# Kernel tuning notes

Hardware: AMD Instinct MI355X
Metric: run time of the kernel (lower is better)

## Reference

```python
import jax, jax.numpy as jnp
import numpy as np

N_FILES = 256      # number of files (segments)
LINES = 128        # lines per file
T = N_FILES * LINES  # total lines = 32768
D_ENC = 768        # CodeBERT hidden size
HID = 256          # GCN hidden_dim
SD = 128           # shared_dim
PD = 128           # private_dim
WINDOW = 2         # line-graph window
S_AM = 30.0        # AM-Softmax scale
M_AM = 0.35        # AM-Softmax margin


def _build_edges():
    # build_line_graph: connect lines within a file at offsets 1..WINDOW, both directions
    idx = np.arange(T)
    srcs, dsts = [], []
    for off in range(1, WINDOW + 1):
        m = (idx % LINES) + off < LINES  # j stays inside the same file
        i = idx[m]; j = i + off
        srcs += [i, j]; dsts += [j, i]
    return np.stack([np.concatenate(srcs), np.concatenate(dsts)]).astype(np.int32)


def setup_inputs() -> dict:
    key = jax.random.key(0)
    ks = jax.random.split(key, 18)
    std = 0.02
    inp = {
        "line_emb": jax.random.normal(ks[0], (T, D_ENC), jnp.float32),
        "W1": jax.random.normal(ks[1], (D_ENC, HID), jnp.float32) * std,
        "b1": jnp.zeros((HID,), jnp.float32),
        "W2": jax.random.normal(ks[2], (HID, HID), jnp.float32) * std,
        "b2": jnp.zeros((HID,), jnp.float32),
        "attn_w": jax.random.normal(ks[3], (HID, 1), jnp.float32) * std,
        "attn_b": jnp.zeros((1,), jnp.float32),
        "Ws": jax.random.normal(ks[4], (HID, SD), jnp.float32) * std,
        "bs": jnp.zeros((SD,), jnp.float32),
        "Wp": jax.random.normal(ks[5], (HID, PD), jnp.float32) * std,
        "bp": jnp.zeros((PD,), jnp.float32),
        "cls_w": jax.random.normal(ks[6], (SD, 2), jnp.float32) * std,
        "Wd1": jax.random.normal(ks[7], (SD, SD), jnp.float32) * std,
        "bd1": jnp.zeros((SD,), jnp.float32),
        "Wd2": jax.random.normal(ks[8], (SD, 2), jnp.float32) * std,
        "bd2": jnp.zeros((2,), jnp.float32),
        "line_ptr": jnp.arange(0, T + 1, LINES, dtype=jnp.int32),
        "edge_index": jnp.asarray(_build_edges()),
        "file_labels": jax.random.randint(ks[9], (N_FILES,), 0, 2, jnp.int32),
    }
    return inp


def _l2norm(x):
    return x / jnp.maximum(jnp.linalg.norm(x, axis=1, keepdims=True), 1e-12)


def _gcn(x, W, b, src, dst, n):
    sl = jnp.arange(n, dtype=src.dtype)
    src = jnp.concatenate([src, sl]); dst = jnp.concatenate([dst, sl])
    deg = jax.ops.segment_sum(jnp.ones_like(src, jnp.float32), dst, num_segments=n)
    norm = jax.lax.rsqrt(deg[src] * deg[dst])  # [E+n]
    h = x @ W                                   # [n, out]
    msg = h[src] * norm[:, None]
    return jax.ops.segment_sum(msg, dst, num_segments=n) + b


def reference(line_emb, W1, b1, W2, b2, attn_w, attn_b, Ws, bs, Wp, bp,
              cls_w, Wd1, bd1, Wd2, bd2, line_ptr, edge_index, file_labels):
    n = line_emb.shape[0]
    n_files = line_ptr.shape[0] - 1
    src, dst = edge_index[0], edge_index[1]

    h = jax.nn.relu(_gcn(line_emb, W1, b1, src, dst, n))
    h = _gcn(h, W2, b2, src, dst, n)               # [T, HID]

    # ragged per-file softmax attention pooling
    seg = jnp.searchsorted(line_ptr, jnp.arange(n, dtype=line_ptr.dtype), side="right") - 1
    logits = (h @ attn_w).squeeze(-1) + attn_b[0]  # [T]
    seg_max = jax.ops.segment_max(logits, seg, num_segments=n_files)
    e = jnp.exp(logits - seg_max[seg])
    denom = jax.ops.segment_sum(e, seg, num_segments=n_files)
    att_weights = e / denom[seg]
    h_file = jax.ops.segment_sum(att_weights[:, None] * h, seg, num_segments=n_files)  # [N, HID]

    # disentangle heads
    z_shared = h_file @ Ws + bs
    z_private = h_file @ Wp + bp

    # AM-Softmax classifier (labels given -> subtract margin on true class)
    cos = _l2norm(z_shared) @ (cls_w / jnp.maximum(jnp.linalg.norm(cls_w, axis=0, keepdims=True), 1e-12))
    onehot = jax.nn.one_hot(file_labels, 2, dtype=cos.dtype)
    logits_cls = S_AM * (cos - M_AM * onehot)

    # orthogonality loss
    corr = _l2norm(z_shared).T @ _l2norm(z_private)
    ortho = jnp.linalg.norm(corr)

    # domain discriminator (GRL is identity in forward)
    domain_logits = jax.nn.relu(z_shared @ Wd1 + bd1) @ Wd2 + bd2

    return (logits_cls, h_file, z_shared, z_private, att_weights, domain_logits, ortho)
```

## Files before the change

### kernel.cpp

```cpp
#include <hip/hip_runtime.h>


typedef __attribute__((ext_vector_type(8))) short bf16x8;
typedef __attribute__((ext_vector_type(4))) short bf16x4;
typedef __attribute__((ext_vector_type(4))) float f32x4;
typedef __attribute__((ext_vector_type(8))) float f32x8;

__device__ __forceinline__ unsigned short f2bf(float f) {
  union { float f; unsigned int i; } v; v.f = f;
  unsigned int r = v.i + 0x7FFFu + ((v.i >> 16) & 1u);
  return (unsigned short)(r >> 16);
}
__device__ __forceinline__ float bf2f(unsigned short u) {
  union { unsigned int i; float f; } v; v.i = ((unsigned int)u) << 16; return v.f;
}
__device__ __forceinline__ float cvt4dot(bf16x4 v, f32x4* o) {
  (*o)[0] = bf2f(((unsigned short*)&v)[0]); (*o)[1] = bf2f(((unsigned short*)&v)[1]);
  (*o)[2] = bf2f(((unsigned short*)&v)[2]); (*o)[3] = bf2f(((unsigned short*)&v)[3]);
  return 0.f;
}
__device__ __forceinline__ int degf(int p) {
  return 5 - (p < 2 ? 2 - p : 0) - (p > 125 ? p - 125 : 0);
}
__device__ __forceinline__ float wsum(float v) {
#pragma unroll
  for (int o = 1; o < 64; o <<= 1) v += __shfl_xor(v, o);
  return v;
}

__global__ void prep_weights(const float* __restrict__ W1, const float* __restrict__ W2,
                             const float* __restrict__ Ws, const float* __restrict__ Wp,
                             const float* __restrict__ Wd1,
                             unsigned short* __restrict__ W1t, unsigned short* __restrict__ W2t,
                             unsigned short* __restrict__ WsbG, unsigned short* __restrict__ WpbG,
                             unsigned short* __restrict__ Wd1bG) {
  __shared__ float tile[32][33];
  int id = blockIdx.x;
  int tx = threadIdx.x, ty = threadIdx.y;
  if (id >= 256) {
    int id2 = id - 256;
    const float* src; unsigned short* dst; int blk;
    if (id2 < 32)      { src = Ws;  dst = WsbG;  blk = id2; }
    else if (id2 < 64) { src = Wp;  dst = WpbG;  blk = id2 - 32; }
    else               { src = Wd1; dst = Wd1bG; blk = id2 - 64; }
    int tid = ty * 32 + tx;
    int e0 = blk * 1024 + tid * 4;
    f32x4 v = *(const f32x4*)&src[e0];
    unsigned short o[4];
#pragma unroll
    for (int j = 0; j < 4; ++j) o[j] = f2bf(v[j]);
    *(bf16x4*)&dst[e0] = *(bf16x4*)o;
    return;
  }
  const float* src; unsigned short* dst; int R, C, bx, by;
  if (id < 192) { src = W1; dst = W1t; R = 768; C = 256; bx = (id % 8) * 32; by = (id / 8) * 32; }
  else { id -= 192; src = W2; dst = W2t; R = 256; C = 256; bx = (id % 8) * 32; by = (id / 8) * 32; }
#pragma unroll
  for (int j = 0; j < 32; j += 8)
    tile[ty + j][tx] = src[(by + ty + j) * C + bx + tx];
  __syncthreads();
#pragma unroll
  for (int j = 0; j < 32; j += 8)
    dst[(bx + ty + j) * R + by + tx] = f2bf(tile[tx][ty + j]);
}

__global__ __launch_bounds__(1024) void mega(const float* __restrict__ A,
    const unsigned short* __restrict__ W1t, const float* __restrict__ b1,
    const unsigned short* __restrict__ W2t, const float* __restrict__ b2,
    const float* __restrict__ attn_w, const float* __restrict__ attn_b,
    const unsigned short* __restrict__ WsbG, const float* __restrict__ bs,
    const unsigned short* __restrict__ WpbG, const float* __restrict__ bp,
    const float* __restrict__ cls_w, const int* __restrict__ labels,
    const unsigned short* __restrict__ Wd1bG, const float* __restrict__ bd1,
    const float* __restrict__ Wd2, const float* __restrict__ bd2,
    float* __restrict__ out) {
  __shared__ __align__(16) char lds[131072];
  unsigned short* sA1 = (unsigned short*)lds;
  unsigned short* sB1 = (unsigned short*)(lds + 32768);
  unsigned short* H1  = (unsigned short*)lds;
  unsigned short* G1L = (unsigned short*)(lds + 65536);
  unsigned short* sB2 = (unsigned short*)lds;
  unsigned short* H2  = (unsigned short*)lds;
  unsigned short* hB  = (unsigned short*)(lds + 65536);
  unsigned short* Wlo = (unsigned short*)lds;
  unsigned short* Whi = (unsigned short*)(lds + 65536);
  __shared__ float awS[256];
  __shared__ float lgS[128];
  __shared__ float redM[64];
  __shared__ float scr[1024];
  __shared__ float hfS[256];
  __shared__ float zsS[128], znS[128];
  __shared__ float redS[16];

  const int t = threadIdx.x;
  const int wave = t >> 6, lane = t & 63;
  const int wr = wave >> 2, wc = wave & 3;
  const int file = blockIdx.x;
  const long rowA = (long)file * 128;

  if (t < 256) awS[t] = attn_w[t];

  f32x4 acc[2][4];
#pragma unroll
  for (int m = 0; m < 2; ++m)
#pragma unroll
    for (int n = 0; n < 4; ++n) acc[m][n] = (f32x4)0.0f;

  const int arow = t >> 3, acol = (t & 7) * 8;
  const int aswz = arow * 64 + (acol ^ ((arow & 7) << 3));
  f32x8 areg;
#define ISSUE_A1(kt) areg = *(const f32x8*)&A[(rowA + arow) * 768 + (kt) * 64 + acol]
#define WRITE_A1(buf) { unsigned short u[8];                                      \
    _Pragma("unroll") for (int j = 0; j < 8; ++j) u[j] = f2bf(areg[j]);           \
    *(bf16x8*)&sA1[(buf) * 8192 + aswz] = *(bf16x8*)u; }
#define ISSUE_B1(kt, buf) _Pragma("unroll") for (int it = 0; it < 2; ++it) {      \
    int flat = (it * 1024 + t) * 8;                                               \
    int n = flat >> 6, k = flat & 63;                                             \
    const unsigned short* g = W1t + n * 768 + (kt) * 64 + (k ^ ((n & 7) << 3));   \
    __builtin_amdgcn_global_load_lds(                                             \
        (const __attribute__((address_space(1))) unsigned int*)g,                 \
        (__attribute__((address_space(3))) unsigned int*)                         \
            &sB1[(buf) * 16384 + (it * 16 + wave) * 512], 16, 0, 0); }

  ISSUE_A1(0); ISSUE_B1(0, 0); WRITE_A1(0);
  __syncthreads();
  for (int kt = 0; kt < 12; ++kt) {
    const int cur = kt & 1, nxt = cur ^ 1;
    if (kt + 1 < 12) { ISSUE_A1(kt + 1); ISSUE_B1(kt + 1, nxt); }
#pragma unroll
    for (int kk = 0; kk < 2; ++kk) {
      const int kb = kk * 32 + (lane >> 4) * 8;
      bf16x8 af[2], bfr[4];
#pragma unroll
      for (int m = 0; m < 2; ++m) {
        int r = wr * 32 + m * 16 + (lane & 15);
        af[m] = *(const bf16x8*)&sA1[cur * 8192 + r * 64 + (kb ^ ((r & 7) << 3))];
      }
#pragma unroll
      for (int n = 0; n < 4; ++n) {
        int r = wc * 64 + n * 16 + (lane & 15);
        bfr[n] = *(const bf16x8*)&sB1[cur * 16384 + r * 64 + (kb ^ ((r & 7) << 3))];
      }
#pragma unroll
      for (int m = 0; m < 2; ++m)
#pragma unroll
        for (int n = 0; n < 4; ++n)
          acc[m][n] = __builtin_amdgcn_mfma_f32_16x16x32_bf16(af[m], bfr[n], acc[m][n], 0, 0, 0);
    }
    if (kt + 1 < 12) WRITE_A1(nxt);
    __syncthreads();
  }
#pragma unroll
  for (int m = 0; m < 2; ++m)
#pragma unroll
    for (int n = 0; n < 4; ++n) {
      int r = wr * 32 + m * 16 + (lane >> 4) * 4;
      int c = wc * 64 + n * 16 + (lane & 15);
#pragma unroll
      for (int j = 0; j < 4; ++j) H1[(r + j) * 256 + c] = f2bf(acc[m][n][j]);
    }
  __syncthreads();
#pragma unroll
  for (int it = 0; it < 8; ++it) {
    int g = it * 1024 + t;
    int l = g >> 6, c0 = (g & 63) * 4;
    int dl = degf(l);
    f32x4 s = (f32x4)0.0f;
#pragma unroll
    for (int o = -2; o <= 2; ++o) {
      int q = l + o;
      if (q < 0 || q > 127) continue;
      float w = __frsqrt_rn((float)(dl * degf(q)));
      bf16x4 hv4 = *(const bf16x4*)&H1[q * 256 + c0];
      f32x4 hv; cvt4dot(hv4, &hv);
      s += w * hv;
    }
    f32x4 b = *(const f32x4*)&b1[c0];
    unsigned short o4[4];
#pragma unroll
    for (int j = 0; j < 4; ++j) o4[j] = f2bf(fmaxf(s[j] + b[j], 0.f));
    *(bf16x4*)&G1L[l * 256 + (c0 ^ ((l & 7) << 3))] = *(bf16x4*)o4;
  }
  __syncthreads();

#pragma unroll
  for (int m = 0; m < 2; ++m)
#pragma unroll
    for (int n = 0; n < 4; ++n) acc[m][n] = (f32x4)0.0f;
#define ISSUE_B2(kt, buf) _Pragma("unroll") for (int it = 0; it < 2; ++it) {      \
    int flat = (it * 1024 + t) * 8;                                               \
    int n = flat >> 6, k = flat & 63;                                             \
    const unsigned short* g = W2t + n * 256 + (kt) * 64 + (k ^ ((n & 7) << 3));   \
    __builtin_amdgcn_global_load_lds(                                             \
        (const __attribute__((address_space(1))) unsigned int*)g,                 \
        (__attribute__((address_space(3))) unsigned int*)                         \
            &sB2[(buf) * 16384 + (it * 16 + wave) * 512], 16, 0, 0); }

  ISSUE_B2(0, 0);
  __syncthreads();
  for (int kt = 0; kt < 4; ++kt) {
    const int cur = kt & 1, nxt = cur ^ 1;
    if (kt + 1 < 4) ISSUE_B2(kt + 1, nxt);
#pragma unroll
    for (int kk = 0; kk < 2; ++kk) {
      const int kb = kk * 32 + (lane >> 4) * 8;
      bf16x8 af[2], bfr[4];
#pragma unroll
      for (int m = 0; m < 2; ++m) {
        int r = wr * 32 + m * 16 + (lane & 15);
        int col = kt * 64 + kb;
        af[m] = *(const bf16x8*)&G1L[r * 256 + (col ^ ((r & 7) << 3))];
      }
#pragma unroll
      for (int n = 0; n < 4; ++n) {
        int r = wc * 64 + n * 16 + (lane & 15);
        bfr[n] = *(const bf16x8*)&sB2[cur * 16384 + r * 64 + (kb ^ ((r & 7) << 3))];
      }
#pragma unroll
      for (int m = 0; m < 2; ++m)
#pragma unroll
        for (int n = 0; n < 4; ++n)
          acc[m][n] = __builtin_amdgcn_mfma_f32_16x16x32_bf16(af[m], bfr[n], acc[m][n], 0, 0, 0);
    }
    __syncthreads();
  }
#pragma unroll
  for (int m = 0; m < 2; ++m)
#pragma unroll
    for (int n = 0; n < 4; ++n) {
      int r = wr * 32 + m * 16 + (lane >> 4) * 4;
      int c = wc * 64 + n * 16 + (lane & 15);
#pragma unroll
      for (int j = 0; j < 4; ++j) H2[(r + j) * 256 + c] = f2bf(acc[m][n][j]);
    }
  __syncthreads();
#pragma unroll
  for (int it = 0; it < 8; ++it) {
    int g = it * 1024 + t;
    int l = g >> 6, c0 = (g & 63) * 4;
    int dl = degf(l);
    f32x4 s = (f32x4)0.0f;
#pragma unroll
    for (int o = -2; o <= 2; ++o) {
      int q = l + o;
      if (q < 0 || q > 127) continue;
      float w = __frsqrt_rn((float)(dl * degf(q)));
      bf16x4 hv4 = *(const bf16x4*)&H2[q * 256 + c0];
      f32x4 hv; cvt4dot(hv4, &hv);
      s += w * hv;
    }
    f32x4 b = *(const f32x4*)&b2[c0];
    unsigned short o4[4];
#pragma unroll
    for (int j = 0; j < 4; ++j) o4[j] = f2bf(s[j] + b[j]);
    *(bf16x4*)&hB[l * 256 + c0] = *(bf16x4*)o4;
  }
  __syncthreads();
#define ISSUE_WB(srcG, dstL, rounds) _Pragma("unroll") for (int it = 0; it < (rounds); ++it) { \
    const unsigned short* g = (srcG) + (it * 1024 + t) * 8;                        \
    __builtin_amdgcn_global_load_lds(                                              \
        (const __attribute__((address_space(1))) unsigned int*)g,                  \
        (__attribute__((address_space(3))) unsigned int*)                          \
            &(dstL)[(it * 16 + wave) * 512], 16, 0, 0); }
  ISSUE_WB(WsbG, Wlo, 4);

  {
    int l = t >> 3, p = t & 7;
    float part = 0.f;
#pragma unroll 4
    for (int j = 0; j < 32; ++j) {
      int c = p * 32 + ((j + 4 * p + l) & 31);
      part += bf2f(hB[l * 256 + c]) * awS[c];
    }
    part += __shfl_xor(part, 1);
    part += __shfl_xor(part, 2);
    part += __shfl_xor(part, 4);
    if (p == 0) lgS[l] = part + attn_b[0];
  }
  __syncthreads();
  if (t < 64) redM[t] = fmaxf(lgS[t], lgS[t + 64]);
  __syncthreads();
  for (int s = 32; s > 0; s >>= 1) {
    if (t < s) redM[t] = fmaxf(redM[t], redM[t + s]);
    __syncthreads();
  }
  float mx = redM[0];
  __syncthreads();
  if (t < 128) lgS[t] = expf(lgS[t] - mx);
  __syncthreads();
  if (t < 64) redM[t] = lgS[t] + lgS[t + 64];
  __syncthreads();
  for (int s = 32; s > 0; s >>= 1) {
    if (t < s) redM[t] += redM[t + s];
    __syncthreads();
  }
  float dn = redM[0];
  __syncthreads();
  if (t < 128) {
    float w = lgS[t] / dn;
    lgS[t] = w;
    out[131584 + file * 128 + t] = w;
  }
  __syncthreads();
  {
    int c = t & 255, grp = t >> 8;
    float s = 0.f;
    for (int l = grp * 32; l < grp * 32 + 32; ++l) s += lgS[l] * bf2f(hB[l * 256 + c]);
    scr[grp * 256 + c] = s;
  }
  __syncthreads();
  if (t < 256) {
    float tot = scr[t] + scr[256 + t] + scr[512 + t] + scr[768 + t];
    hfS[t] = tot;
    out[512 + file * 256 + t] = tot;
  }
  __syncthreads();

  ISSUE_WB(WpbG, Whi, 4);
  {
    int g = t >> 7, j = t & 127;
    float s = 0.f;
#pragma unroll 8
    for (int c = g * 32; c < g * 32 + 32; ++c) s += hfS[c] * bf2f(Wlo[c * 128 + j]);
    scr[g * 128 + j] = s;
  }
  __syncthreads();
  ISSUE_WB(Wd1bG, Wlo, 2);
  if (t < 128) {
    float zs = bs[t];
#pragma unroll
    for (int g = 0; g < 8; ++g) zs += scr[g * 128 + t];
    zsS[t] = zs;
    out[66048 + file * 128 + t] = zs;
    float s = wsum(zs * zs);
    if (lane == 0) redS[wave] = s;
  }
  __syncthreads();
  if (t == 0) redS[8] = fmaxf(sqrtf(redS[0] + redS[1]), 1e-12f);
  {
    int g = t >> 7, j = t & 127;
    float s = 0.f;
#pragma unroll 8
    for (int c = g * 32; c < g * 32 + 32; ++c) s += hfS[c] * bf2f(Whi[c * 128 + j]);
    scr[g * 128 + j] = s;
  }
  __syncthreads();
  if (t < 128) {
    znS[t] = zsS[t] / redS[8];
  } else if (t < 256) {
    int j = t - 128;
    float zp = bp[j];
#pragma unroll
    for (int g = 0; g < 8; ++g) zp += scr[g * 128 + j];
    out[98816 + file * 128 + j] = zp;
  }
  __syncthreads();
  {
    int j = t & 127;
    if (t < 512) {
      float v;
      if (t < 128)       v = znS[j] * cls_w[j * 2 + 0];
      else if (t < 256)  v = znS[j] * cls_w[j * 2 + 1];
      else if (t < 384)  { float w0 = cls_w[j * 2 + 0]; v = w0 * w0; }
      else               { float w1 = cls_w[j * 2 + 1]; v = w1 * w1; }
      float s = wsum(v);
      if (lane == 0) redS[wave] = s;
    }
  }
  __syncthreads();
  if (t == 0) {
    float d0 = redS[0] + redS[1], d1 = redS[2] + redS[3];
    float n0 = fmaxf(sqrtf(redS[4] + redS[5]), 1e-12f);
    float n1 = fmaxf(sqrtf(redS[6] + redS[7]), 1e-12f);
    int lab = labels[file];
    out[file * 2 + 0] = 30.0f * (d0 / n0 - 0.35f * (lab == 0 ? 1.f : 0.f));
    out[file * 2 + 1] = 30.0f * (d1 / n1 - 0.35f * (lab == 1 ? 1.f : 0.f));
  }
  __syncthreads();
  {
    int g = t >> 7, j = t & 127;
    float s = 0.f;
#pragma unroll 8
    for (int a = g * 16; a < g * 16 + 16; ++a) s += zsS[a] * bf2f(Wlo[a * 128 + j]);
    scr[g * 128 + j] = s;
  }
  __syncthreads();
  if (t < 128) {
    float dd = bd1[t];
#pragma unroll
    for (int g = 0; g < 8; ++g) dd += scr[g * 128 + t];
    dd = fmaxf(dd, 0.f);
    float s0 = wsum(dd * Wd2[t * 2 + 0]);
    if (lane == 0) redS[wave] = s0;
    float s1 = wsum(dd * Wd2[t * 2 + 1]);
    if (lane == 0) redS[4 + wave] = s1;
  }
  __syncthreads();
  if (t == 0) {
    out[164352 + file * 2 + 0] = redS[0] + redS[1] + bd2[0];
    out[164352 + file * 2 + 1] = redS[4] + redS[5] + bd2[1];
  }
#undef ISSUE_A1
#undef WRITE_A1
#undef ISSUE_B1
#undef ISSUE_B2
#undef ISSUE_WB
}

__global__ __launch_bounds__(128) void znorm(const float* __restrict__ out,
                                             float* __restrict__ zsn,
                                             float* __restrict__ zpn) {
  const int f = blockIdx.x, j = threadIdx.x;
  __shared__ float red[128];
  float zs = out[66048 + f * 128 + j];
  float zp = out[98816 + f * 128 + j];
  red[j] = zs * zs; __syncthreads();
  for (int s = 64; s > 0; s >>= 1) { if (j < s) red[j] += red[j + s]; __syncthreads(); }
  float ns = sqrtf(red[0]); __syncthreads();
  zsn[f * 128 + j] = zs / fmaxf(ns, 1e-12f);
  red[j] = zp * zp; __syncthreads();
  for (int s = 64; s > 0; s >>= 1) { if (j < s) red[j] += red[j + s]; __syncthreads(); }
  float np = sqrtf(red[0]); __syncthreads();
  zpn[f * 128 + j] = zp / fmaxf(np, 1e-12f);
}

__global__ __launch_bounds__(128) void ortho_partial(const float* __restrict__ zsn,
                                                     const float* __restrict__ zpn,
                                                     float* __restrict__ partial) {
  const int a = blockIdx.x, b = threadIdx.x;
  float s = 0.f;
  for (int f = 0; f < 256; ++f) s += zsn[f * 128 + a] * zpn[f * 128 + b];
  __shared__ float red[128];
  red[b] = s * s; __syncthreads();
  for (int st = 64; st > 0; st >>= 1) { if (b < st) red[b] += red[b + st]; __syncthreads(); }
  if (b == 0) partial[a] = red[0];
}

__global__ __launch_bounds__(128) void ortho_final(const float* __restrict__ partial,
                                                   float* __restrict__ out) {
  const int t = threadIdx.x;
  __shared__ float red[128];
  red[t] = partial[t]; __syncthreads();
  for (int st = 64; st > 0; st >>= 1) { if (t < st) red[t] += red[t + st]; __syncthreads(); }
  if (t == 0) out[164864] = sqrtf(red[0]);
}

extern "C" void kernel_launch(void* const* d_in, const int* in_sizes, int n_in,
                              void* d_out, int out_size, void* d_ws, size_t ws_size,
                              hipStream_t stream) {
  const float* line_emb = (const float*)d_in[0];
  const float* W1     = (const float*)d_in[1];
  const float* b1     = (const float*)d_in[2];
  const float* W2     = (const float*)d_in[3];
  const float* b2     = (const float*)d_in[4];
  const float* attn_w = (const float*)d_in[5];
  const float* attn_b = (const float*)d_in[6];
  const float* Ws     = (const float*)d_in[7];
  const float* bs     = (const float*)d_in[8];
  const float* Wp     = (const float*)d_in[9];
  const float* bp     = (const float*)d_in[10];
  const float* cls_w  = (const float*)d_in[11];
  const float* Wd1    = (const float*)d_in[12];
  const float* bd1    = (const float*)d_in[13];
  const float* Wd2    = (const float*)d_in[14];
  const float* bd2    = (const float*)d_in[15];
  const int* labels   = (const int*)d_in[18];

  char* ws = (char*)d_ws;
  unsigned short* W1t  = (unsigned short*)(ws + 0);
  unsigned short* W2t  = (unsigned short*)(ws + 393216);
  float* zsn           = (float*)(ws + 524288);
  float* zpn           = (float*)(ws + 655360);
  float* partial       = (float*)(ws + 786432);
  unsigned short* WsbG = (unsigned short*)(ws + 1048576);
  unsigned short* WpbG = (unsigned short*)(ws + 1114112);
  unsigned short* Wd1bG= (unsigned short*)(ws + 1179648);
  float* out           = (float*)d_out;

  prep_weights<<<dim3(336), dim3(32, 8), 0, stream>>>(W1, W2, Ws, Wp, Wd1,
                                                      W1t, W2t, WsbG, WpbG, Wd1bG);
  mega<<<dim3(256), dim3(1024), 0, stream>>>(line_emb, W1t, b1, W2t, b2,
                                             attn_w, attn_b, WsbG, bs, WpbG, bp,
                                             cls_w, labels, Wd1bG, bd1, Wd2, bd2, out);
  znorm<<<dim3(256), dim3(128), 0, stream>>>(out, zsn, zpn);
  ortho_partial<<<dim3(128), dim3(128), 0, stream>>>(zsn, zpn, partial);
  ortho_final<<<dim3(1), dim3(128), 0, stream>>>(partial, out);
}
```

Measured before the change: 73.18 us.

## Fuse z normalisation into mega kernel, swizzle hB, and use wave-shuffle reductions

```diff
diff --git a/kernel.cpp b/kernel.cpp
--- a/kernel.cpp
+++ b/kernel.cpp
@@ -73,6 +73,7 @@
     const float* __restrict__ cls_w, const int* __restrict__ labels,
     const unsigned short* __restrict__ Wd1bG, const float* __restrict__ bd1,
     const float* __restrict__ Wd2, const float* __restrict__ bd2,
+    float* __restrict__ zsn_g, float* __restrict__ zpn_g,
     float* __restrict__ out) {
   __shared__ __align__(16) char lds[131072];
   unsigned short* sA1 = (unsigned short*)lds;
@@ -86,10 +87,10 @@
   unsigned short* Whi = (unsigned short*)(lds + 65536);
   __shared__ float awS[256];
   __shared__ float lgS[128];
-  __shared__ float redM[64];
+  __shared__ float redM[4];
   __shared__ float scr[1024];
   __shared__ float hfS[256];
-  __shared__ float zsS[128], znS[128];
+  __shared__ float zsS[128], zpS[128], znS[128];
   __shared__ float redS[16];
 
   const int t = threadIdx.x;
@@ -253,7 +254,7 @@
     unsigned short o4[4];
 #pragma unroll
     for (int j = 0; j < 4; ++j) o4[j] = f2bf(s[j] + b[j]);
-    *(bf16x4*)&hB[l * 256 + c0] = *(bf16x4*)o4;
+    *(bf16x4*)&hB[l * 256 + (c0 ^ ((l & 7) << 3))] = *(bf16x4*)o4;
   }
   __syncthreads();
 #define ISSUE_WB(srcG, dstL, rounds) _Pragma("unroll") for (int it = 0; it < (rounds); ++it) { \
@@ -266,11 +267,14 @@
 
   {
     int l = t >> 3, p = t & 7;
+    const int sw = (l & 7) << 3;
     float part = 0.f;
-#pragma unroll 4
-    for (int j = 0; j < 32; ++j) {
-      int c = p * 32 + ((j + 4 * p + l) & 31);
-      part += bf2f(hB[l * 256 + c]) * awS[c];
+#pragma unroll
+    for (int j = 0; j < 4; ++j) {
+      int c0 = p * 32 + j * 8;
+      bf16x8 hv = *(const bf16x8*)&hB[l * 256 + (c0 ^ sw)];
+#pragma unroll
+      for (int e = 0; e < 8; ++e) part += bf2f(((unsigned short*)&hv)[e]) * awS[c0 + e];
     }
     part += __shfl_xor(part, 1);
     part += __shfl_xor(part, 2);
@@ -278,24 +282,22 @@
     if (p == 0) lgS[l] = part + attn_b[0];
   }
   __syncthreads();
-  if (t < 64) redM[t] = fmaxf(lgS[t], lgS[t + 64]);
-  __syncthreads();
-  for (int s = 32; s > 0; s >>= 1) {
-    if (t < s) redM[t] = fmaxf(redM[t], redM[t + s]);
-    __syncthreads();
-  }
+  if (wave == 0) {
+    float m0 = fmaxf(lgS[lane], lgS[lane + 64]);
+#pragma unroll
+    for (int o = 1; o < 64; o <<= 1) m0 = fmaxf(m0, __shfl_xor(m0, o));
+    if (lane == 0) redM[0] = m0;
+  }
+  __syncthreads();
   float mx = redM[0];
-  __syncthreads();
   if (t < 128) lgS[t] = expf(lgS[t] - mx);
   __syncthreads();
-  if (t < 64) redM[t] = lgS[t] + lgS[t + 64];
-  __syncthreads();
-  for (int s = 32; s > 0; s >>= 1) {
-    if (t < s) redM[t] += redM[t + s];
-    __syncthreads();
-  }
-  float dn = redM[0];
-  __syncthreads();
+  if (wave == 0) {
+    float s0 = wsum(lgS[lane] + lgS[lane + 64]);
+    if (lane == 0) redM[1] = s0;
+  }
+  __syncthreads();
+  float dn = redM[1];
   if (t < 128) {
     float w = lgS[t] / dn;
     lgS[t] = w;
@@ -305,7 +307,8 @@
   {
     int c = t & 255, grp = t >> 8;
     float s = 0.f;
-    for (int l = grp * 32; l < grp * 32 + 32; ++l) s += lgS[l] * bf2f(hB[l * 256 + c]);
+    for (int l = grp * 32; l < grp * 32 + 32; ++l)
+      s += lgS[l] * bf2f(hB[l * 256 + (c ^ ((l & 7) << 3))]);
     scr[grp * 256 + c] = s;
   }
   __syncthreads();
@@ -346,13 +349,41 @@
   }
   __syncthreads();
   if (t < 128) {
-    znS[t] = zsS[t] / redS[8];
+    float zsn = zsS[t] / redS[8];
+    znS[t] = zsn;
+    zsn_g[file * 128 + t] = zsn;
   } else if (t < 256) {
     int j = t - 128;
     float zp = bp[j];
 #pragma unroll
     for (int g = 0; g < 8; ++g) zp += scr[g * 128 + j];
+    zpS[j] = zp;
     out[98816 + file * 128 + j] = zp;
+    float s = wsum(zp * zp);
+    if (lane == 0) redS[wave] = s;
+  }
+  __syncthreads();
+  if (t == 0) redS[9] = fmaxf(sqrtf(redS[2] + redS[3]), 1e-12f);
+  __syncthreads();
+  if (t < 128) zpn_g[file * 128 + t] = zpS[t] / redS[9];
+  {
+    int j = t & 127;
+    if (t >= 128 && t < 640) {
+      int tt = t - 128;
+      float v;
+      if (tt < 128)       v = znS[j] * cls_w[j * 2 + 0];
+      else if (tt < 256)  v = znS[j] * cls_w[j * 2 + 1];
+      else if (tt < 384)  { float w0 = cls_w[j * 2 + 0]; v = w0 * w0; }
+      else                { float w1 = cls_w[j * 2 + 1]; v = w1 * w1; }
+      float s = wsum(v);
+      if (lane == 0) redS[4 + (tt >> 7)] = s;
+    }
+  }
+  __syncthreads();
+  if (t == 0) {
+    float d0 = redS[4] + ((lane == 0) ? 0.f : 0.f), dd0, dd1;
+    dd0 = 0.f; dd1 = 0.f;
+    (void)d0;
   }
   __syncthreads();
   {
@@ -407,33 +438,27 @@
 #undef ISSUE_WB
 }
 
-__global__ __launch_bounds__(128) void znorm(const float* __restrict__ out,
-                                             float* __restrict__ zsn,
-                                             float* __restrict__ zpn) {
-  const int f = blockIdx.x, j = threadIdx.x;
-  __shared__ float red[128];
-  float zs = out[66048 + f * 128 + j];
-  float zp = out[98816 + f * 128 + j];
-  red[j] = zs * zs; __syncthreads();
-  for (int s = 64; s > 0; s >>= 1) { if (j < s) red[j] += red[j + s]; __syncthreads(); }
-  float ns = sqrtf(red[0]); __syncthreads();
-  zsn[f * 128 + j] = zs / fmaxf(ns, 1e-12f);
-  red[j] = zp * zp; __syncthreads();
-  for (int s = 64; s > 0; s >>= 1) { if (j < s) red[j] += red[j + s]; __syncthreads(); }
-  float np = sqrtf(red[0]); __syncthreads();
-  zpn[f * 128 + j] = zp / fmaxf(np, 1e-12f);
-}
-
-__global__ __launch_bounds__(128) void ortho_partial(const float* __restrict__ zsn,
+__global__ __launch_bounds__(256) void ortho_partial(const float* __restrict__ zsn,
                                                      const float* __restrict__ zpn,
                                                      float* __restrict__ partial) {
-  const int a = blockIdx.x, b = threadIdx.x;
+  const int a = blockIdx.x;
+  const int b = threadIdx.x & 127, half = threadIdx.x >> 7;
   float s = 0.f;
-  for (int f = 0; f < 256; ++f) s += zsn[f * 128 + a] * zpn[f * 128 + b];
-  __shared__ float red[128];
-  red[b] = s * s; __syncthreads();
-  for (int st = 64; st > 0; st >>= 1) { if (b < st) red[b] += red[b + st]; __syncthreads(); }
-  if (b == 0) partial[a] = red[0];
+  for (int f = half * 128; f < half * 128 + 128; ++f)
+    s += zsn[f * 128 + a] * zpn[f * 128 + b];
+  __shared__ float sc[256];
+  sc[half * 128 + b] = s;
+  __syncthreads();
+  if (threadIdx.x < 128) {
+    float v = sc[threadIdx.x] + sc[128 + threadIdx.x];
+    sc[threadIdx.x] = v * v;
+  }
+  __syncthreads();
+  for (int st = 64; st > 0; st >>= 1) {
+    if (threadIdx.x < st) sc[threadIdx.x] += sc[threadIdx.x + st];
+    __syncthreads();
+  }
+  if (threadIdx.x == 0) partial[a] = sc[0];
 }
 
 __global__ __launch_bounds__(128) void ortho_final(const float* __restrict__ partial,
@@ -481,8 +506,8 @@
                                                       W1t, W2t, WsbG, WpbG, Wd1bG);
   mega<<<dim3(256), dim3(1024), 0, stream>>>(line_emb, W1t, b1, W2t, b2,
                                              attn_w, attn_b, WsbG, bs, WpbG, bp,
-                                             cls_w, labels, Wd1bG, bd1, Wd2, bd2, out);
-  znorm<<<dim3(256), dim3(128), 0, stream>>>(out, zsn, zpn);
-  ortho_partial<<<dim3(128), dim3(128), 0, stream>>>(zsn, zpn, partial);
+                                             cls_w, labels, Wd1bG, bd1, Wd2, bd2,
+                                             zsn, zpn, out);
+  ortho_partial<<<dim3(128), dim3(256), 0, stream>>>(zsn, zpn, partial);
   ortho_final<<<dim3(1), dim3(128), 0, stream>>>(partial, out);
 }
```

Result: slower. 94.28 us (+28.8%).
